# Kernel optimization log

Hardware: AMD Instinct MI355X
Metric: run time of the kernel (lower is better)

## Reference

```python
import jax, jax.numpy as jnp
import numpy as np
import math

B, N, C, A, H = 1, 320, 128, 32, 4  # batch, n_res, rep_2d channels, attn channels, heads


def _layernorm(x, w, b, eps=1e-5):
    mu = jnp.mean(x, axis=-1, keepdims=True)
    var = jnp.var(x, axis=-1, keepdims=True)
    return (x - mu) * jax.lax.rsqrt(var + eps) * w + b


def setup_inputs() -> dict:
    key = jax.random.key(0)
    ks = jax.random.split(key, 12)
    s = 0.02
    return {
        "x2d": jax.random.normal(ks[0], (B, N, N, C), dtype=jnp.float32),
        "mask": jnp.ones((B, N, N), dtype=jnp.float32),
        "norm_w": jnp.ones((C,), dtype=jnp.float32),
        "norm_b": jnp.zeros((C,), dtype=jnp.float32),
        "Wq": jax.random.normal(ks[1], (C, A * H), dtype=jnp.float32) * s,
        "Wk": jax.random.normal(ks[2], (C, A * H), dtype=jnp.float32) * s,
        "Wv": jax.random.normal(ks[3], (C, A * H), dtype=jnp.float32) * s,
        "Wb": jax.random.normal(ks[4], (C, H), dtype=jnp.float32) * s,
        "Wg": jax.random.normal(ks[5], (C, A * H), dtype=jnp.float32) * s,
        "bg": jnp.zeros((A * H,), dtype=jnp.float32),
        "Wo": jax.random.normal(ks[6], (A * H, C), dtype=jnp.float32) * s,
        "bo": jnp.zeros((C,), dtype=jnp.float32),
    }


def reference(x2d, mask, norm_w, norm_b, Wq, Wk, Wv, Wb, Wg, bg, Wo, bo):
    xn = _layernorm(x2d, norm_w, norm_b)                      # [B,N,N,C]
    # note: torch .view(..., A, H) splits the output channel as (A, H)
    q = (xn @ Wq).reshape(B, N, N, A, H)
    k = (xn @ Wk).reshape(B, N, N, A, H)
    v = (xn @ Wv).reshape(B, N, N, A, H)
    b = xn @ Wb                                               # [B,N,N,H] -> b[b,j,k,h]
    g = jax.nn.sigmoid((xn @ Wg + bg).reshape(B, N, N, A, H))
    w = jnp.einsum('bijch,bikch->bijkh', q, k) / math.sqrt(A)
    # torch: b.unsqueeze(1).transpose(2,3) => w[b,i,j,k,h] += b[b,k,j,h]
    w = w + jnp.transpose(b, (0, 2, 1, 3))[:, None]           # [B,1,N,N,H]
    w = (w + 100.0) * mask[:, :, None, :, None] - 100.0
    w = jax.nn.softmax(w, axis=-2)                            # over k
    out = jnp.einsum('bijkh,bikch->bijch', w, v) * g          # [B,N,N,A,H]
    out = out.reshape(B, N, N, A * H) @ Wo + bo               # [B,N,N,C]
    out = out * mask[..., None]
    return out
```

## Files before the change

kernel.cpp:

```cpp
#include <hip/hip_runtime.h>
#include <hip/hip_bf16.h>
#include <math.h>

#define N 320
#define C 128
#define A 32
#define H 4
#define NPOS (N*N)

typedef __attribute__((ext_vector_type(8))) __bf16 bf16x8;
typedef __attribute__((ext_vector_type(16))) float f32x16;

union frag_u { int4 i; bf16x8 v; unsigned u[4]; };

#define MFMA32(va, vb, vc) __builtin_amdgcn_mfma_f32_32x32x16_bf16((va), (vb), (vc), 0, 0, 0)

#define WAVE_LDS_FENCE() do { \
    asm volatile("s_waitcnt lgkmcnt(0)" ::: "memory"); \
    __builtin_amdgcn_sched_barrier(0); \
} while (0)

static __device__ __forceinline__ unsigned pk_bf16(float lo, float hi) {
    union { __hip_bfloat162 h; unsigned u; } cv;
    cv.h = __float22bfloat162_rn(make_float2(lo, hi));
    return cv.u;
}

static __device__ __forceinline__ float bf16_to_f32(unsigned short u) {
    union { unsigned u; float f; } c;
    c.u = ((unsigned)u) << 16;
    return c.f;
}

static __device__ __forceinline__ float u32_as_f32(unsigned u) {
    union { unsigned u; float f; } c;
    c.u = u;
    return c.f;
}

__global__ __launch_bounds__(256)
void wprep_kernel(const float* __restrict__ Wq,
                  const float* __restrict__ Wk,
                  const float* __restrict__ Wv,
                  const float* __restrict__ Wg,
                  const float* __restrict__ Wo,
                  unsigned short* __restrict__ WF) {
    const float isq = 0.17677669529663687f;
    int tid = blockIdx.x * 256 + threadIdx.x;
    int lane = tid & 63;
    int kk = (tid >> 6) & 7;
    int ct = (tid >> 9) & 3;
    int mat = tid >> 11;
    const float* src = (mat == 0) ? Wq : (mat == 1) ? Wk : (mat == 2) ? Wv
                     : (mat == 3) ? Wg : Wo;
    float scl = (mat == 0) ? isq : 1.0f;
    int col = ct * 32 + (lane & 31);
    int c0 = kk * 16 + (lane >> 5) * 8;
    float v[8];
    #pragma unroll
    for (int e = 0; e < 8; e++) {
        int rr = c0 + e;
        int srow = (mat == 4) ? (((rr & 31) << 2) | (rr >> 5)) : rr;
        v[e] = src[(size_t)srow * 128 + col] * scl;
    }
    int4 out;
    out.x = pk_bf16(v[0], v[1]);
    out.y = pk_bf16(v[2], v[3]);
    out.z = pk_bf16(v[4], v[5]);
    out.w = pk_bf16(v[6], v[7]);
    *(int4*)((char*)WF + (size_t)tid * 16) = out;
}

__global__ __launch_bounds__(256)
void btrans_kernel(const float* __restrict__ Bp, unsigned short* __restrict__ BpTb) {
    __shared__ float tile[64][65];
    const int b = blockIdx.x;
    const int h = b / 25;
    const int bk = (b % 25) / 5;
    const int bj = b % 5;
    const int k0 = bk * 64, j0 = bj * 64;
    const float* src = Bp + (size_t)h * NPOS;
    unsigned short* dst = BpTb + (size_t)h * NPOS;
    const int t = threadIdx.x;
    #pragma unroll
    for (int u = 0; u < 16; ++u) {
        int idx = u * 256 + t;
        int kk = idx >> 6, jj = idx & 63;
        tile[kk][jj] = src[(size_t)(k0 + kk) * N + j0 + jj];
    }
    __syncthreads();
    #pragma unroll
    for (int u = 0; u < 16; ++u) {
        int idx = u * 256 + t;
        int jj = idx >> 6, kk = idx & 63;
        dst[(size_t)(j0 + jj) * N + k0 + kk] =
            (unsigned short)(pk_bf16(tile[kk][jj], 0.f) & 0xffffu);
    }
}

__global__ __launch_bounds__(256)
void ln_proj_kernel(const float* __restrict__ x2d,
                    const float* __restrict__ norm_w,
                    const float* __restrict__ norm_b,
                    const float* __restrict__ Wb,
                    const float* __restrict__ bg,
                    const unsigned short* __restrict__ WF,
                    unsigned short* __restrict__ Qb,
                    unsigned short* __restrict__ Kb,
                    unsigned short* __restrict__ Vta,
                    unsigned short* __restrict__ Gb,
                    float* __restrict__ Bp) {
    __shared__ __align__(16) unsigned char shbuf[16896];
    unsigned char* xnb = shbuf;

    const int t = threadIdx.x;
    const int gpos0 = blockIdx.x * 32;

    {
        const int r = t >> 3, s = t & 7;
        const float4* src = (const float4*)(x2d + (size_t)(gpos0 + r) * 128 + s * 16);
        float4 xv[4];
        #pragma unroll
        for (int u = 0; u < 4; u++) xv[u] = src[u];
        float sum = 0.f, sq = 0.f;
        #pragma unroll
        for (int u = 0; u < 4; u++) {
            sum += xv[u].x + xv[u].y + xv[u].z + xv[u].w;
            sq += xv[u].x * xv[u].x + xv[u].y * xv[u].y
                + xv[u].z * xv[u].z + xv[u].w * xv[u].w;
        }
        sum += __shfl_xor(sum, 1); sum += __shfl_xor(sum, 2); sum += __shfl_xor(sum, 4);
        sq  += __shfl_xor(sq, 1);  sq  += __shfl_xor(sq, 2);  sq  += __shfl_xor(sq, 4);
        float mean = sum * (1.0f / 128.0f);
        float var  = sq * (1.0f / 128.0f) - mean * mean;
        float rstd = rsqrtf(var + 1e-5f);

        const float4* wsrc = (const float4*)(norm_w + s * 16);
        const float4* bsrc = (const float4*)(norm_b + s * 16);
        const float4* wb4  = (const float4*)Wb;
        float pb0 = 0.f, pb1 = 0.f, pb2 = 0.f, pb3 = 0.f;
        float4 xe;
        #pragma unroll
        for (int u = 0; u < 4; u++) {
            float4 wv = wsrc[u], bv = bsrc[u], x4 = xv[u];
            float4 xn;
            xn.x = (x4.x - mean) * rstd * wv.x + bv.x;
            xn.y = (x4.y - mean) * rstd * wv.y + bv.y;
            xn.z = (x4.z - mean) * rstd * wv.z + bv.z;
            xn.w = (x4.w - mean) * rstd * wv.w + bv.w;
            int cb = s * 16 + u * 4;
            float4 w0 = wb4[cb + 0], w1 = wb4[cb + 1], w2 = wb4[cb + 2], w3 = wb4[cb + 3];
            pb0 = fmaf(xn.x, w0.x, fmaf(xn.y, w1.x, fmaf(xn.z, w2.x, fmaf(xn.w, w3.x, pb0))));
            pb1 = fmaf(xn.x, w0.y, fmaf(xn.y, w1.y, fmaf(xn.z, w2.y, fmaf(xn.w, w3.y, pb1))));
            pb2 = fmaf(xn.x, w0.z, fmaf(xn.y, w1.z, fmaf(xn.z, w2.z, fmaf(xn.w, w3.z, pb2))));
            pb3 = fmaf(xn.x, w0.w, fmaf(xn.y, w1.w, fmaf(xn.z, w2.w, fmaf(xn.w, w3.w, pb3))));
            if (u & 1) {
                int g = s * 2 + (u >> 1);
                int4 gr;
                gr.x = pk_bf16(xe.x, xe.y);
                gr.y = pk_bf16(xe.z, xe.w);
                gr.z = pk_bf16(xn.x, xn.y);
                gr.w = pk_bf16(xn.z, xn.w);
                *(int4*)(xnb + r * 256 + ((g ^ (r & 7)) << 4)) = gr;
            } else {
                xe = xn;
            }
        }
        pb0 += __shfl_xor(pb0, 1); pb0 += __shfl_xor(pb0, 2); pb0 += __shfl_xor(pb0, 4);
        pb1 += __shfl_xor(pb1, 1); pb1 += __shfl_xor(pb1, 2); pb1 += __shfl_xor(pb1, 4);
        pb2 += __shfl_xor(pb2, 1); pb2 += __shfl_xor(pb2, 2); pb2 += __shfl_xor(pb2, 4);
        pb3 += __shfl_xor(pb3, 1); pb3 += __shfl_xor(pb3, 2); pb3 += __shfl_xor(pb3, 4);
        if (s < 4) {
            float pbsel = (s == 0) ? pb0 : (s == 1) ? pb1 : (s == 2) ? pb2 : pb3;
            Bp[(size_t)s * NPOS + gpos0 + r] = pbsel;
        }
    }
    __syncthreads();

    const int lane = t & 63;
    const int w = t >> 6;
    const int col = lane & 31;
    const int hi = lane >> 5;

    frag_u af[8];
    #pragma unroll
    for (int kk = 0; kk < 8; kk++)
        af[kk].i = *(const int4*)(xnb + col * 256 + (((kk * 2 + hi) ^ (col & 7)) << 4));
    __syncthreads();

    const char* wf = (const char*)WF + (size_t)w * 4 * 8 * 1024;
    float* stage_w = (float*)shbuf + w * 1056;

    for (int ct = 0; ct < 4; ct++) {
        f32x16 acc;
        #pragma unroll
        for (int r = 0; r < 16; r++) acc[r] = 0.f;
        #pragma unroll
        for (int kk = 0; kk < 8; kk++) {
            frag_u bf;
            bf.i = *(const int4*)(wf + (ct * 8 + kk) * 1024 + lane * 16);
            acc = MFMA32(af[kk].v, bf.v, acc);
        }
        #pragma unroll
        for (int r = 0; r < 16; r++) {
            int patr = (r & 3) + 8 * (r >> 2) + 4 * hi;
            stage_w[col * 33 + patr] = acc[r];
        }
        WAVE_LDS_FENCE();
        if (w < 2) {
            char* dst = (w == 0) ? (char*)Qb : (char*)Kb;
            #pragma unroll
            for (int h = 0; h < 4; h++) {
                float f[4];
                #pragma unroll
                for (int e = 0; e < 4; e++)
                    f[e] = stage_w[((hi * 4 + e) * 4 + h) * 33 + col];
                uint2 val;
                val.x = pk_bf16(f[0], f[1]);
                val.y = pk_bf16(f[2], f[3]);
                *(uint2*)(dst + ((size_t)(h * 4 + ct) * NPOS + gpos0 + col) * 16 + hi * 8) = val;
            }
        } else if (w == 2) {
            int cc = col, half = hi;
            int plane = (cc & 3) * 32 + ct * 8 + (cc >> 2);
            unsigned pk[8];
            #pragma unroll
            for (int j2 = 0; j2 < 8; j2++)
                pk[j2] = pk_bf16(stage_w[cc * 33 + half * 16 + 2 * j2],
                                 stage_w[cc * 33 + half * 16 + 2 * j2 + 1]);
            int4* dst = (int4*)((char*)Vta + ((size_t)plane * NPOS + gpos0 + half * 16) * 2);
            dst[0] = make_int4(pk[0], pk[1], pk[2], pk[3]);
            dst[1] = make_int4(pk[4], pk[5], pk[6], pk[7]);
        } else {
            #pragma unroll
            for (int h = 0; h < 4; h++) {
                float f[4];
                #pragma unroll
                for (int e = 0; e < 4; e++) {
                    float z = stage_w[((hi * 4 + e) * 4 + h) * 33 + col]
                            + bg[ct * 32 + (hi * 4 + e) * 4 + h];
                    f[e] = 1.0f / (1.0f + __expf(-z));
                }
                uint2 val;
                val.x = pk_bf16(f[0], f[1]);
                val.y = pk_bf16(f[2], f[3]);
                *(uint2*)((char*)Gb + ((size_t)(h * 4 + ct) * NPOS + gpos0 + col) * 16 + hi * 8) = val;
            }
        }
        WAVE_LDS_FENCE();
    }
}

__global__ __launch_bounds__(320, 2)
void attn_kernel(const unsigned short* __restrict__ Qb,
                 const unsigned short* __restrict__ Kb,
                 const unsigned short* __restrict__ Vta,
                 const unsigned short* __restrict__ Gb,
                 const unsigned short* __restrict__ BpTb,
                 const float* __restrict__ mask,
                 unsigned short* __restrict__ Ob) {
    __shared__ __align__(16) unsigned char smem[21120];
    __shared__ float mparr[320];
    __shared__ float m2arr[320];

    const int i = blockIdx.x >> 2;
    const int h = blockIdx.x & 3;
    const int t = threadIdx.x;
    const int lane = t & 63;
    const int w = t >> 6;
    const int col = lane & 31;
    const int hi = lane >> 5;
    const int jt0 = w * 64;

    frag_u qf[2][2];
    const char* qplane = (const char*)Qb + ((size_t)(h * 4) * NPOS + (size_t)i * N) * 16;
    #pragma unroll
    for (int jt = 0; jt < 2; ++jt) {
        int jrow = jt0 + jt * 32 + col;
        #pragma unroll
        for (int cf = 0; cf < 2; ++cf) {
            int g = cf * 2 + hi;
            qf[jt][cf].i = *(const int4*)(qplane + ((size_t)g * NPOS + jrow) * 16);
        }
    }

    const char* kpl = (const char*)Kb + ((size_t)(h * 4) * NPOS + (size_t)i * N) * 16;

    const char* vbsrc = (const char*)Vta + ((size_t)h * 32 * NPOS + (size_t)i * N) * 2;
    #pragma unroll
    for (int it = 0; it < 4; ++it) {
        int tt = t + it * 320;
        int a = tt / 40, kg = tt % 40;
        int4 val = *(const int4*)(vbsrc + (size_t)a * NPOS * 2 + kg * 16);
        *(int4*)(smem + a * 640 + ((kg ^ (a & 7)) << 4)) = val;
    }
    {
        int kt_ = t >> 5, hi_ = (t >> 4) & 1, r_ = t & 15;
        int k = kt_ * 32 + (r_ & 3) + 8 * (r_ >> 2) + 4 * hi_;
        float m_ = mask[(size_t)i * N + k];
        mparr[t] = m_;
        m2arr[t] = fmaf(100.f, m_, -100.f);
    }

    frag_u kf0, kf1, kf0n, kf1n;
    kf0.i = *(const int4*)(kpl + ((size_t)hi * NPOS + col) * 16);
    kf1.i = *(const int4*)(kpl + ((size_t)(2 + hi) * NPOS + col) * 16);
    f32x16 S0, S1;
    #pragma unroll
    for (int r = 0; r < 16; ++r) { S0[r] = 0.f; S1[r] = 0.f; }
    S0 = MFMA32(kf0.v, qf[0][0].v, S0);
    S0 = MFMA32(kf1.v, qf[0][1].v, S0);
    S1 = MFMA32(kf0.v, qf[1][0].v, S1);
    S1 = MFMA32(kf1.v, qf[1][1].v, S1);
    kf0n.i = *(const int4*)(kpl + ((size_t)hi * NPOS + 32 + col) * 16);
    kf1n.i = *(const int4*)(kpl + ((size_t)(2 + hi) * NPOS + 32 + col) * 16);

    const unsigned short* br0 = BpTb + (size_t)h * NPOS + (size_t)(jt0 + col) * N + 4 * hi;
    const unsigned short* br1 = br0 + (size_t)32 * N;
    uint2 b0[4], b1[4];
    #pragma unroll
    for (int q = 0; q < 4; ++q) b0[q] = *(const uint2*)(br0 + 8 * q);
    #pragma unroll
    for (int q = 0; q < 4; ++q) b1[q] = *(const uint2*)(br1 + 8 * q);

    __syncthreads();

    f32x16 accO[2];
    #pragma unroll
    for (int r = 0; r < 16; ++r) { accO[0][r] = 0.f; accO[1][r] = 0.f; }
    float lsum[2] = { 0.f, 0.f };

    for (int kt = 0; kt < 10; ++kt) {
        const int kbase = kt * 32;

        frag_u vf0, vf1;
        vf0.i = *(const int4*)(smem + col * 640 + (((kt * 4 + 0 + hi) ^ (col & 7)) << 4));
        vf1.i = *(const int4*)(smem + col * 640 + (((kt * 4 + 2 + hi) ^ (col & 7)) << 4));

        float4 mk4[4], m2v[4];
        const float* mp  = mparr + kbase + hi * 16;
        const float* m2p = m2arr + kbase + hi * 16;
        #pragma unroll
        for (int q = 0; q < 4; ++q) {
            mk4[q] = *(const float4*)(mp + 4 * q);
            m2v[q] = *(const float4*)(m2p + 4 * q);
        }

        uint2 bn0[4], bn1[4];
        if (kt < 9) {
            #pragma unroll
            for (int q = 0; q < 4; ++q) bn0[q] = *(const uint2*)(br0 + kbase + 32 + 8 * q);
            #pragma unroll
            for (int q = 0; q < 4; ++q) bn1[q] = *(const uint2*)(br1 + kbase + 32 + 8 * q);
        }

        float sv0[16], sv1[16];
        #pragma unroll
        for (int q = 0; q < 4; ++q) {
            float a0 = u32_as_f32(b0[q].x << 16);
            float a1 = u32_as_f32(b0[q].x & 0xffff0000u);
            float a2 = u32_as_f32(b0[q].y << 16);
            float a3 = u32_as_f32(b0[q].y & 0xffff0000u);
            sv0[4*q+0] = fmaf(S0[4*q+0] + a0, mk4[q].x, m2v[q].x);
            sv0[4*q+1] = fmaf(S0[4*q+1] + a1, mk4[q].y, m2v[q].y);
            sv0[4*q+2] = fmaf(S0[4*q+2] + a2, mk4[q].z, m2v[q].z);
            sv0[4*q+3] = fmaf(S0[4*q+3] + a3, mk4[q].w, m2v[q].w);
            float c0 = u32_as_f32(b1[q].x << 16);
            float c1 = u32_as_f32(b1[q].x & 0xffff0000u);
            float c2 = u32_as_f32(b1[q].y << 16);
            float c3 = u32_as_f32(b1[q].y & 0xffff0000u);
            sv1[4*q+0] = fmaf(S1[4*q+0] + c0, mk4[q].x, m2v[q].x);
            sv1[4*q+1] = fmaf(S1[4*q+1] + c1, mk4[q].y, m2v[q].y);
            sv1[4*q+2] = fmaf(S1[4*q+2] + c2, mk4[q].z, m2v[q].z);
            sv1[4*q+3] = fmaf(S1[4*q+3] + c3, mk4[q].w, m2v[q].w);
        }

        if (kt < 9) {
            f32x16 t0, t1;
            #pragma unroll
            for (int r = 0; r < 16; ++r) { t0[r] = 0.f; t1[r] = 0.f; }
            __builtin_amdgcn_s_setprio(1);
            t0 = MFMA32(kf0n.v, qf[0][0].v, t0);
            t0 = MFMA32(kf1n.v, qf[0][1].v, t0);
            t1 = MFMA32(kf0n.v, qf[1][0].v, t1);
            t1 = MFMA32(kf1n.v, qf[1][1].v, t1);
            __builtin_amdgcn_s_setprio(0);
            S0 = t0;
            S1 = t1;
            kf0 = kf0n;
            kf1 = kf1n;
            if (kt < 8) {
                int krn = kbase + 64 + col;
                kf0n.i = *(const int4*)(kpl + ((size_t)hi * NPOS + krn) * 16);
                kf1n.i = *(const int4*)(kpl + ((size_t)(2 + hi) * NPOS + krn) * 16);
            }
        }

        float pe0[16], pe1[16];
        float l00 = 0.f, l01 = 0.f, l02 = 0.f, l03 = 0.f;
        float l10 = 0.f, l11 = 0.f, l12 = 0.f, l13 = 0.f;
        #pragma unroll
        for (int q = 0; q < 4; ++q) {
            pe0[4*q+0] = __expf(sv0[4*q+0]); pe0[4*q+1] = __expf(sv0[4*q+1]);
            pe0[4*q+2] = __expf(sv0[4*q+2]); pe0[4*q+3] = __expf(sv0[4*q+3]);
            pe1[4*q+0] = __expf(sv1[4*q+0]); pe1[4*q+1] = __expf(sv1[4*q+1]);
            pe1[4*q+2] = __expf(sv1[4*q+2]); pe1[4*q+3] = __expf(sv1[4*q+3]);
            l00 += pe0[4*q+0]; l01 += pe0[4*q+1]; l02 += pe0[4*q+2]; l03 += pe0[4*q+3];
            l10 += pe1[4*q+0]; l11 += pe1[4*q+1]; l12 += pe1[4*q+2]; l13 += pe1[4*q+3];
        }
        lsum[0] += (l00 + l01) + (l02 + l03);
        lsum[1] += (l10 + l11) + (l12 + l13);

        frag_u bfA0, bfA1, bfB0, bfB1;
        {
            unsigned p[8];
            #pragma unroll
            for (int q = 0; q < 8; ++q) p[q] = pk_bf16(pe0[2*q], pe0[2*q+1]);
            unsigned x0 = p[0], y0 = p[2], x1 = p[1], y1 = p[3];
            unsigned x2 = p[4], y2 = p[6], x3 = p[5], y3 = p[7];
            asm("v_permlane32_swap_b32 %0, %1" : "+v"(x0), "+v"(y0));
            asm("v_permlane32_swap_b32 %0, %1" : "+v"(x1), "+v"(y1));
            asm("v_permlane32_swap_b32 %0, %1" : "+v"(x2), "+v"(y2));
            asm("v_permlane32_swap_b32 %0, %1" : "+v"(x3), "+v"(y3));
            bfA0.u[0] = x0; bfA0.u[1] = x1; bfA0.u[2] = y0; bfA0.u[3] = y1;
            bfA1.u[0] = x2; bfA1.u[1] = x3; bfA1.u[2] = y2; bfA1.u[3] = y3;
        }
        {
            unsigned p[8];
            #pragma unroll
            for (int q = 0; q < 8; ++q) p[q] = pk_bf16(pe1[2*q], pe1[2*q+1]);
            unsigned x0 = p[0], y0 = p[2], x1 = p[1], y1 = p[3];
            unsigned x2 = p[4], y2 = p[6], x3 = p[5], y3 = p[7];
            asm("v_permlane32_swap_b32 %0, %1" : "+v"(x0), "+v"(y0));
            asm("v_permlane32_swap_b32 %0, %1" : "+v"(x1), "+v"(y1));
            asm("v_permlane32_swap_b32 %0, %1" : "+v"(x2), "+v"(y2));
            asm("v_permlane32_swap_b32 %0, %1" : "+v"(x3), "+v"(y3));
            bfB0.u[0] = x0; bfB0.u[1] = x1; bfB0.u[2] = y0; bfB0.u[3] = y1;
            bfB1.u[0] = x2; bfB1.u[1] = x3; bfB1.u[2] = y2; bfB1.u[3] = y3;
        }

        __builtin_amdgcn_s_setprio(1);
        accO[0] = MFMA32(vf0.v, bfA0.v, accO[0]);
        accO[0] = MFMA32(vf1.v, bfA1.v, accO[0]);
        accO[1] = MFMA32(vf0.v, bfB0.v, accO[1]);
        accO[1] = MFMA32(vf1.v, bfB1.v, accO[1]);
        __builtin_amdgcn_s_setprio(0);

        if (kt < 9) {
            #pragma unroll
            for (int q = 0; q < 4; ++q) { b0[q] = bn0[q]; b1[q] = bn1[q]; }
        }
    }

    __syncthreads();
    float* st = (float*)(smem + w * 4224);
    const char* gplane = (const char*)Gb + ((size_t)(h * 4) * NPOS + (size_t)i * N) * 16;

    #pragma unroll
    for (int jt = 0; jt < 2; ++jt) {
        float lt = lsum[jt] + __shfl_xor(lsum[jt], 32);
        float inv = 1.0f / lt;
        #pragma unroll
        for (int r = 0; r < 16; ++r) {
            const int a = (r & 3) + 8 * (r >> 2) + 4 * hi;
            st[col * 33 + a] = accO[jt][r] * inv;
        }
        WAVE_LDS_FENCE();
        {
            int jj = lane & 31;
            int ah0 = hi * 16;
            int jrow = jt0 + jt * 32 + jj;
            int4 g0 = *(const int4*)(gplane + ((size_t)(2 * hi + 0) * NPOS + jrow) * 16);
            int4 g1 = *(const int4*)(gplane + ((size_t)(2 * hi + 1) * NPOS + jrow) * 16);
            unsigned gw[8] = { (unsigned)g0.x, (unsigned)g0.y, (unsigned)g0.z, (unsigned)g0.w,
                               (unsigned)g1.x, (unsigned)g1.y, (unsigned)g1.z, (unsigned)g1.w };
            unsigned pk8[8];
            #pragma unroll
            for (int e = 0; e < 8; ++e) {
                float ge0 = bf16_to_f32((unsigned short)(gw[e] & 0xffffu));
                float ge1 = bf16_to_f32((unsigned short)(gw[e] >> 16));
                pk8[e] = pk_bf16(st[jj * 33 + ah0 + 2 * e + 0] * ge0,
                                 st[jj * 33 + ah0 + 2 * e + 1] * ge1);
            }
            char* dst = (char*)Ob + (((size_t)i * N + jrow) * 128 + h * 32 + ah0) * 2;
            *(int4*)dst = make_int4(pk8[0], pk8[1], pk8[2], pk8[3]);
            *(int4*)(dst + 16) = make_int4(pk8[4], pk8[5], pk8[6], pk8[7]);
        }
        WAVE_LDS_FENCE();
    }
}

__global__ __launch_bounds__(256)
void outproj_kernel(const unsigned short* __restrict__ Ob,
                    const unsigned short* __restrict__ WoF,
                    const float* __restrict__ bo,
                    const float* __restrict__ mask,
                    float* __restrict__ out) {
    __shared__ __align__(16) unsigned char obs[64 * 256];
    __shared__ float stage[4][32 * 65];

    const int t = threadIdx.x;
    const int gpos0 = blockIdx.x * 64;

    {
        const int r = t >> 2, s = t & 3;
        const char* src = (const char*)Ob + ((size_t)(gpos0 + r) * 128 + s * 32) * 2;
        #pragma unroll
        for (int u = 0; u < 4; ++u) {
            int4 v = *(const int4*)(src + u * 16);
            int g = s * 4 + u;
            *(int4*)(obs + r * 256 + ((g ^ (r & 7)) << 4)) = v;
        }
    }
    __syncthreads();

    const int lane = t & 63;
    const int w = t >> 6;
    const int col = lane & 31;
    const int hi = lane >> 5;

    f32x16 acc0, acc1;
    float bocol = bo[w * 32 + col];
    #pragma unroll
    for (int r = 0; r < 16; ++r) { acc0[r] = bocol; acc1[r] = bocol; }

    const char* wf = (const char*)WoF + (size_t)w * 8 * 1024;
    #pragma unroll
    for (int kk = 0; kk < 8; ++kk) {
        frag_u bf, a0, a1;
        bf.i = *(const int4*)(wf + kk * 1024 + lane * 16);
        int row0 = col, row1 = 32 + col;
        a0.i = *(const int4*)(obs + row0 * 256 + (((kk * 2 + hi) ^ (row0 & 7)) << 4));
        a1.i = *(const int4*)(obs + row1 * 256 + (((kk * 2 + hi) ^ (row1 & 7)) << 4));
        acc0 = MFMA32(a0.v, bf.v, acc0);
        acc1 = MFMA32(a1.v, bf.v, acc1);
    }

    float* st = stage[w];
    #pragma unroll
    for (int r = 0; r < 16; ++r) {
        int patr = (r & 3) + 8 * (r >> 2) + 4 * hi;
        st[col * 65 + patr] = acc0[r];
        st[col * 65 + 32 + patr] = acc1[r];
    }
    WAVE_LDS_FENCE();
    {
        int row = lane;
        float mv = mask[gpos0 + row];
        float4* dst = (float4*)(out + (size_t)(gpos0 + row) * 128 + w * 32);
        #pragma unroll
        for (int u = 0; u < 8; ++u) {
            float4 o;
            o.x = st[(4 * u + 0) * 65 + row] * mv;
            o.y = st[(4 * u + 1) * 65 + row] * mv;
            o.z = st[(4 * u + 2) * 65 + row] * mv;
            o.w = st[(4 * u + 3) * 65 + row] * mv;
            dst[u] = o;
        }
    }
}

extern "C" void kernel_launch(void* const* d_in, const int* in_sizes, int n_in,
                              void* d_out, int out_size, void* d_ws, size_t ws_size,
                              hipStream_t stream) {
    const float* x2d    = (const float*)d_in[0];
    const float* mask   = (const float*)d_in[1];
    const float* norm_w = (const float*)d_in[2];
    const float* norm_b = (const float*)d_in[3];
    const float* Wq     = (const float*)d_in[4];
    const float* Wk     = (const float*)d_in[5];
    const float* Wv     = (const float*)d_in[6];
    const float* Wb     = (const float*)d_in[7];
    const float* Wg     = (const float*)d_in[8];
    const float* bg     = (const float*)d_in[9];
    const float* Wo     = (const float*)d_in[10];
    const float* bo     = (const float*)d_in[11];
    float* out = (float*)d_out;

    char* ws = (char*)d_ws;
    float* Bp  = (float*)ws;                                   ws += (size_t)H * NPOS * 4;
    unsigned short* BpTb = (unsigned short*)ws;                ws += (size_t)H * NPOS * 4;
    unsigned short* Qb  = (unsigned short*)ws;                 ws += (size_t)NPOS * C * 2;
    unsigned short* Kb  = (unsigned short*)ws;                 ws += (size_t)NPOS * C * 2;
    unsigned short* Vta = (unsigned short*)ws;                 ws += (size_t)NPOS * C * 2;
    unsigned short* Gb  = (unsigned short*)ws;                 ws += (size_t)NPOS * C * 2;
    unsigned short* Ob  = (unsigned short*)ws;                 ws += (size_t)NPOS * C * 2;
    unsigned short* WF  = (unsigned short*)ws;
    unsigned short* WoF = WF + (size_t)4 * 16384;

    wprep_kernel<<<40, 256, 0, stream>>>(Wq, Wk, Wv, Wg, Wo, WF);

    ln_proj_kernel<<<NPOS / 32, 256, 0, stream>>>(x2d, norm_w, norm_b, Wb, bg,
                                                  WF, Qb, Kb, Vta, Gb, Bp);

    btrans_kernel<<<H * 25, 256, 0, stream>>>(Bp, BpTb);

    attn_kernel<<<N * H, 320, 0, stream>>>(Qb, Kb, Vta, Gb, BpTb, mask, Ob);

    outproj_kernel<<<NPOS / 64, 256, 0, stream>>>(Ob, WoF, bo, mask, out);
}
```

Measured before the change: 188.5 us.

## Split attention key loop across two wave groups and reduce partials in LDS

The attention block grows from 320 to 640 threads. Each group of five waves now handles half of the key tiles for the same query rows. Partial output accumulators and softmax row sums from the second group are passed through LDS and added into the first group, which then does normalisation, gating and the store. The aim is to halve the serial per-wave key loop and hide more latency, at the cost of extra barriers, an LDS reduction, and a spurious extra MFMA in the prologue.

```diff
diff --git a/kernel.cpp b/kernel.cpp
--- a/kernel.cpp
+++ b/kernel.cpp
@@ -251,7 +251,7 @@
     }
 }
 
-__global__ __launch_bounds__(320, 2)
+__global__ __launch_bounds__(640)
 void attn_kernel(const unsigned short* __restrict__ Qb,
                  const unsigned short* __restrict__ Kb,
                  const unsigned short* __restrict__ Vta,
@@ -262,6 +262,7 @@
     __shared__ __align__(16) unsigned char smem[21120];
     __shared__ float mparr[320];
     __shared__ float m2arr[320];
+    __shared__ float lsumbuf[320];
 
     const int i = blockIdx.x >> 2;
     const int h = blockIdx.x & 3;
@@ -270,7 +271,11 @@
     const int w = t >> 6;
     const int col = lane & 31;
     const int hi = lane >> 5;
-    const int jt0 = w * 64;
+    const int wl = (w >= 5) ? (w - 5) : w;
+    const int jt0 = wl * 64;
+    const int k0 = (w >= 5) ? 5 : 0;
+    const int kend = k0 + 5;
+    const int koff = k0 * 32;
 
     frag_u qf[2][2];
     const char* qplane = (const char*)Qb + ((size_t)(h * 4) * NPOS + (size_t)i * N) * 16;
@@ -288,13 +293,13 @@
 
     const char* vbsrc = (const char*)Vta + ((size_t)h * 32 * NPOS + (size_t)i * N) * 2;
     #pragma unroll
-    for (int it = 0; it < 4; ++it) {
-        int tt = t + it * 320;
+    for (int it = 0; it < 2; ++it) {
+        int tt = t + it * 640;
         int a = tt / 40, kg = tt % 40;
         int4 val = *(const int4*)(vbsrc + (size_t)a * NPOS * 2 + kg * 16);
         *(int4*)(smem + a * 640 + ((kg ^ (a & 7)) << 4)) = val;
     }
-    {
+    if (t < 320) {
         int kt_ = t >> 5, hi_ = (t >> 4) & 1, r_ = t & 15;
         int k = kt_ * 32 + (r_ & 3) + 8 * (r_ >> 2) + 4 * hi_;
         float m_ = mask[(size_t)i * N + k];
@@ -303,25 +308,29 @@
     }
 
     frag_u kf0, kf1, kf0n, kf1n;
-    kf0.i = *(const int4*)(kpl + ((size_t)hi * NPOS + col) * 16);
-    kf1.i = *(const int4*)(kpl + ((size_t)(2 + hi) * NPOS + col) * 16);
+    kf0.i = *(const int4*)(kpl + ((size_t)hi * NPOS + koff + col) * 16);
+    kf1.i = *(const int4*)(kpl + ((size_t)(2 + hi) * NPOS + koff + col) * 16);
     f32x16 S0, S1;
     #pragma unroll
     for (int r = 0; r < 16; ++r) { S0[r] = 0.f; S1[r] = 0.f; }
     S0 = MFMA32(kf0.v, qf[0][0].v, S0);
     S0 = MFMA32(kf1.v, qf[0][1].v, S0);
     S1 = MFMA32(kf0.v, qf[1][0].v, S1);
+    S1 = MFMA32(kf0.v, qf[1][1].v, S1);
+    #pragma unroll
+    for (int r = 0; r < 16; ++r) { S1[r] = 0.f; }
+    S1 = MFMA32(kf0.v, qf[1][0].v, S1);
     S1 = MFMA32(kf1.v, qf[1][1].v, S1);
-    kf0n.i = *(const int4*)(kpl + ((size_t)hi * NPOS + 32 + col) * 16);
-    kf1n.i = *(const int4*)(kpl + ((size_t)(2 + hi) * NPOS + 32 + col) * 16);
+    kf0n.i = *(const int4*)(kpl + ((size_t)hi * NPOS + koff + 32 + col) * 16);
+    kf1n.i = *(const int4*)(kpl + ((size_t)(2 + hi) * NPOS + koff + 32 + col) * 16);
 
     const unsigned short* br0 = BpTb + (size_t)h * NPOS + (size_t)(jt0 + col) * N + 4 * hi;
     const unsigned short* br1 = br0 + (size_t)32 * N;
     uint2 b0[4], b1[4];
     #pragma unroll
-    for (int q = 0; q < 4; ++q) b0[q] = *(const uint2*)(br0 + 8 * q);
-    #pragma unroll
-    for (int q = 0; q < 4; ++q) b1[q] = *(const uint2*)(br1 + 8 * q);
+    for (int q = 0; q < 4; ++q) b0[q] = *(const uint2*)(br0 + koff + 8 * q);
+    #pragma unroll
+    for (int q = 0; q < 4; ++q) b1[q] = *(const uint2*)(br1 + koff + 8 * q);
 
     __syncthreads();
 
@@ -330,7 +339,7 @@
     for (int r = 0; r < 16; ++r) { accO[0][r] = 0.f; accO[1][r] = 0.f; }
     float lsum[2] = { 0.f, 0.f };
 
-    for (int kt = 0; kt < 10; ++kt) {
+    for (int kt = k0; kt < kend; ++kt) {
         const int kbase = kt * 32;
 
         frag_u vf0, vf1;
@@ -347,7 +356,7 @@
         }
 
         uint2 bn0[4], bn1[4];
-        if (kt < 9) {
+        if (kt < kend - 1) {
             #pragma unroll
             for (int q = 0; q < 4; ++q) bn0[q] = *(const uint2*)(br0 + kbase + 32 + 8 * q);
             #pragma unroll
@@ -375,7 +384,7 @@
             sv1[4*q+3] = fmaf(S1[4*q+3] + c3, mk4[q].w, m2v[q].w);
         }
 
-        if (kt < 9) {
+        if (kt < kend - 1) {
             f32x16 t0, t1;
             #pragma unroll
             for (int r = 0; r < 16; ++r) { t0[r] = 0.f; t1[r] = 0.f; }
@@ -389,7 +398,7 @@
             S1 = t1;
             kf0 = kf0n;
             kf1 = kf1n;
-            if (kt < 8) {
+            if (kt < kend - 2) {
                 int krn = kbase + 64 + col;
                 kf0n.i = *(const int4*)(kpl + ((size_t)hi * NPOS + krn) * 16);
                 kf1n.i = *(const int4*)(kpl + ((size_t)(2 + hi) * NPOS + krn) * 16);
@@ -446,47 +455,65 @@
         accO[1] = MFMA32(vf1.v, bfB1.v, accO[1]);
         __builtin_amdgcn_s_setprio(0);
 
-        if (kt < 9) {
+        if (kt < kend - 1) {
             #pragma unroll
             for (int q = 0; q < 4; ++q) { b0[q] = bn0[q]; b1[q] = bn1[q]; }
         }
     }
 
+    #pragma unroll
+    for (int jt = 0; jt < 2; ++jt) {
+        __syncthreads();
+        if (w >= 5) {
+            *(f32x16*)(smem + (t - 320) * 64) = accO[jt];
+            lsumbuf[t - 320] = lsum[jt];
+        }
+        __syncthreads();
+        if (w < 5) {
+            f32x16 o = *(const f32x16*)(smem + t * 64);
+            #pragma unroll
+            for (int r = 0; r < 16; ++r) accO[jt][r] += o[r];
+            lsum[jt] += lsumbuf[t];
+        }
+    }
     __syncthreads();
-    float* st = (float*)(smem + w * 4224);
-    const char* gplane = (const char*)Gb + ((size_t)(h * 4) * NPOS + (size_t)i * N) * 16;
-
-    #pragma unroll
-    for (int jt = 0; jt < 2; ++jt) {
-        float lt = lsum[jt] + __shfl_xor(lsum[jt], 32);
-        float inv = 1.0f / lt;
-        #pragma unroll
-        for (int r = 0; r < 16; ++r) {
-            const int a = (r & 3) + 8 * (r >> 2) + 4 * hi;
-            st[col * 33 + a] = accO[jt][r] * inv;
-        }
-        WAVE_LDS_FENCE();
-        {
-            int jj = lane & 31;
-            int ah0 = hi * 16;
-            int jrow = jt0 + jt * 32 + jj;
-            int4 g0 = *(const int4*)(gplane + ((size_t)(2 * hi + 0) * NPOS + jrow) * 16);
-            int4 g1 = *(const int4*)(gplane + ((size_t)(2 * hi + 1) * NPOS + jrow) * 16);
-            unsigned gw[8] = { (unsigned)g0.x, (unsigned)g0.y, (unsigned)g0.z, (unsigned)g0.w,
-                               (unsigned)g1.x, (unsigned)g1.y, (unsigned)g1.z, (unsigned)g1.w };
-            unsigned pk8[8];
-            #pragma unroll
-            for (int e = 0; e < 8; ++e) {
-                float ge0 = bf16_to_f32((unsigned short)(gw[e] & 0xffffu));
-                float ge1 = bf16_to_f32((unsigned short)(gw[e] >> 16));
-                pk8[e] = pk_bf16(st[jj * 33 + ah0 + 2 * e + 0] * ge0,
-                                 st[jj * 33 + ah0 + 2 * e + 1] * ge1);
+
+    if (w < 5) {
+        float* st = (float*)(smem + w * 4224);
+        const char* gplane = (const char*)Gb + ((size_t)(h * 4) * NPOS + (size_t)i * N) * 16;
+
+        #pragma unroll
+        for (int jt = 0; jt < 2; ++jt) {
+            float lt = lsum[jt] + __shfl_xor(lsum[jt], 32);
+            float inv = 1.0f / lt;
+            #pragma unroll
+            for (int r = 0; r < 16; ++r) {
+                const int a = (r & 3) + 8 * (r >> 2) + 4 * hi;
+                st[col * 33 + a] = accO[jt][r] * inv;
             }
-            char* dst = (char*)Ob + (((size_t)i * N + jrow) * 128 + h * 32 + ah0) * 2;
-            *(int4*)dst = make_int4(pk8[0], pk8[1], pk8[2], pk8[3]);
-            *(int4*)(dst + 16) = make_int4(pk8[4], pk8[5], pk8[6], pk8[7]);
-        }
-        WAVE_LDS_FENCE();
+            WAVE_LDS_FENCE();
+            {
+                int jj = lane & 31;
+                int ah0 = hi * 16;
+                int jrow = jt0 + jt * 32 + jj;
+                int4 g0 = *(const int4*)(gplane + ((size_t)(2 * hi + 0) * NPOS + jrow) * 16);
+                int4 g1 = *(const int4*)(gplane + ((size_t)(2 * hi + 1) * NPOS + jrow) * 16);
+                unsigned gw[8] = { (unsigned)g0.x, (unsigned)g0.y, (unsigned)g0.z, (unsigned)g0.w,
+                                   (unsigned)g1.x, (unsigned)g1.y, (unsigned)g1.z, (unsigned)g1.w };
+                unsigned pk8[8];
+                #pragma unroll
+                for (int e = 0; e < 8; ++e) {
+                    float ge0 = bf16_to_f32((unsigned short)(gw[e] & 0xffffu));
+                    float ge1 = bf16_to_f32((unsigned short)(gw[e] >> 16));
+                    pk8[e] = pk_bf16(st[jj * 33 + ah0 + 2 * e + 0] * ge0,
+                                     st[jj * 33 + ah0 + 2 * e + 1] * ge1);
+                }
+                char* dst = (char*)Ob + (((size_t)i * N + jrow) * 128 + h * 32 + ah0) * 2;
+                *(int4*)dst = make_int4(pk8[0], pk8[1], pk8[2], pk8[3]);
+                *(int4*)(dst + 16) = make_int4(pk8[4], pk8[5], pk8[6], pk8[7]);
+            }
+            WAVE_LDS_FENCE();
+        }
     }
 }
 
@@ -595,7 +622,7 @@
 
     btrans_kernel<<<H * 25, 256, 0, stream>>>(Bp, BpTb);
 
-    attn_kernel<<<N * H, 320, 0, stream>>>(Qb, Kb, Vta, Gb, BpTb, mask, Ob);
+    attn_kernel<<<N * H, 640, 0, stream>>>(Qb, Kb, Vta, Gb, BpTb, mask, Ob);
 
     outproj_kernel<<<NPOS / 64, 256, 0, stream>>>(Ob, WoF, bo, mask, out);
 }
```

Measured after the change: 299.3 us. 1.59x slower.
